# Kernel optimization log

Hardware: AMD Instinct MI355X
Metric: run time of the kernel (lower is better)

Reference implementation:

```python
import jax, jax.numpy as jnp
import numpy as np

B, H, W, C = 2, 128, 128, 192
HEADS = 6
HD = C // HEADS
WS = 16
OWIN = int(WS * 0.5) + WS          # 24
PAD = (OWIN - WS) // 2             # 4
NQ = WS * WS
NK = OWIN * OWIN
EPS = 1e-6
HID = ((int(C * 2.667) + 7) // 8) * 8  # 512


def _rel_pos_index():
    cq = np.stack(np.meshgrid(np.arange(WS), np.arange(WS), indexing='ij')).reshape(2, -1)
    ck = np.stack(np.meshgrid(np.arange(OWIN), np.arange(OWIN), indexing='ij')).reshape(2, -1)
    rel = (ck[:, None, :] - cq[:, :, None]).transpose(1, 2, 0).astype(np.int64)  # (nq, nk, 2)
    rel[:, :, 0] += WS - 1
    rel[:, :, 1] += WS - 1
    rel[:, :, 0] *= WS + OWIN - 1
    return rel.sum(-1)  # (nq, nk)

RPI = jnp.asarray(_rel_pos_index())


def setup_inputs() -> dict:
    key = jax.random.key(0)
    ks = jax.random.split(key, 16)
    def w(k, shape, s=0.02):
        return jax.random.normal(k, shape, jnp.float32) * s
    return {
        'x': jax.random.normal(ks[0], (B, H * W, C), jnp.float32),
        'qkv_w': w(ks[1], (3 * C, C)), 'qkv_b': jnp.zeros((3 * C,), jnp.float32),
        'proj_w': w(ks[2], (C, C)), 'proj_b': jnp.zeros((C,), jnp.float32),
        'rpb': w(ks[3], ((WS + OWIN - 1) ** 2, HEADS)),
        'n1_w': jnp.ones((C,), jnp.float32), 'n1_b': jnp.zeros((C,), jnp.float32),
        'ls1': jnp.full((C,), 1e-6, jnp.float32),
        'n2_w': jnp.ones((C,), jnp.float32), 'n2_b': jnp.zeros((C,), jnp.float32),
        'ls2': jnp.full((C,), 1e-6, jnp.float32),
        'fcgv_w': w(ks[4], (2 * HID, C)), 'fcgv_b': jnp.zeros((2 * HID,), jnp.float32),
        'dw_w': w(ks[5], (HID, 1, 3, 3)), 'dw_b': jnp.zeros((HID,), jnp.float32),
        'dwd_w': w(ks[6], (HID, 1, 3, 3)), 'dwd_b': jnp.zeros((HID,), jnp.float32),
        'dil_scale': w(ks[7], (1,), 0.1),
        'fco_w': w(ks[8], (C, HID)), 'fco_b': jnp.zeros((C,), jnp.float32),
    }


def _iln(x, wgt, bias):
    # spatially-holistic LN: stats over (L, C); returns normed x and residual scale
    xf = x.astype(jnp.float32)
    mean = xf.mean(axis=(1, 2), keepdims=True)
    var = ((xf - mean) ** 2).mean(axis=(1, 2), keepdims=True)
    std = jnp.sqrt(var + EPS)
    scale = jnp.minimum(std, 2.0)  # std_ema buffer initialized to 1.0 (eval path)
    xn = (xf - mean) / scale
    return (xn * wgt + bias).astype(x.dtype), scale


def _oca(x, qkv_w, qkv_b, proj_w, proj_b, rpb):
    b = x.shape[0]
    nh, nw = H // WS, W // WS
    nwin = b * nh * nw
    qkv = x @ qkv_w.T + qkv_b
    q, k, v = jnp.split(qkv, 3, axis=-1)
    # non-overlapping query windows: (nwin, heads, nq, hd)
    qw = q.reshape(b, nh, WS, nw, WS, C).transpose(0, 1, 3, 2, 4, 5)
    qw = qw.reshape(nwin, NQ, HEADS, HD).transpose(0, 2, 1, 3)
    # overlapping K/V windows via unfold(kernel=OWIN, stride=WS, pad=PAD)
    kv = jnp.concatenate([k, v], axis=-1).reshape(b, H, W, 2 * C).transpose(0, 3, 1, 2)
    kvp = jnp.pad(kv, ((0, 0), (0, 0), (PAD, PAD), (PAD, PAD)))
    ih = (jnp.arange(nh) * WS)[:, None] + jnp.arange(OWIN)[None, :]
    iw = (jnp.arange(nw) * WS)[:, None] + jnp.arange(OWIN)[None, :]
    kvw = kvp[:, :, ih][:, :, :, :, iw]               # (b, 2C, nh, owin, nw, owin)
    kvw = kvw.transpose(0, 2, 4, 3, 5, 1).reshape(nwin, NK, 2 * C)
    kw = kvw[..., :C].reshape(nwin, NK, HEADS, HD).transpose(0, 2, 1, 3)
    vw = kvw[..., C:].reshape(nwin, NK, HEADS, HD).transpose(0, 2, 1, 3)
    bias = rpb[RPI].transpose(2, 0, 1)                # (heads, nq, nk)
    logits = jnp.einsum('whqd,whkd->whqk', qw, kw) * (HD ** -0.5) + bias
    attn = jax.nn.softmax(logits, axis=-1)
    out = jnp.einsum('whqk,whkd->whqd', attn, vw)
    out = out.transpose(0, 2, 1, 3).reshape(nwin, NQ, C) @ proj_w.T + proj_b
    # window reverse -> (b, H*W, C)
    out = out.reshape(b, nh, nw, WS, WS, C).transpose(0, 1, 3, 2, 4, 5).reshape(b, H * W, C)
    return out


def _dw(x, wgt, bias, dil):
    y = jax.lax.conv_general_dilated(x, wgt, (1, 1), [(dil, dil), (dil, dil)],
                                     rhs_dilation=(dil, dil), feature_group_count=HID)
    return y + bias[None, :, None, None]


def _ffn(x, fcgv_w, fcgv_b, dw_w, dw_b, dwd_w, dwd_b, dil_scale, fco_w, fco_b):
    gv = x @ fcgv_w.T + fcgv_b
    g, val = jnp.split(gv, 2, axis=-1)
    h = jax.nn.silu(g) * val
    h = h.transpose(0, 2, 1).reshape(-1, HID, H, W)
    h = _dw(h, dw_w, dw_b, 1)
    h = h + dil_scale[0] * _dw(h, dwd_w, dwd_b, 2)
    h = h.reshape(-1, HID, H * W).transpose(0, 2, 1)
    return h @ fco_w.T + fco_b


def reference(x, qkv_w, qkv_b, proj_w, proj_b, rpb, n1_w, n1_b, ls1, n2_w, n2_b, ls2,
              fcgv_w, fcgv_b, dw_w, dw_b, dwd_w, dwd_b, dil_scale, fco_w, fco_b):
    xn, std1 = _iln(x, n1_w, n1_b)
    x = x + std1 * (ls1 * _oca(xn, qkv_w, qkv_b, proj_w, proj_b, rpb))
    xn2, std2 = _iln(x, n2_w, n2_b)
    x = x + std2 * (ls2 * _ffn(xn2, fcgv_w, fcgv_b, dw_w, dw_b, dwd_w, dwd_b, dil_scale, fco_w, fco_b))
    return x
```

## Files before the change

### kernel.cpp

```cpp
#include <hip/hip_runtime.h>

#define DI __device__ __forceinline__

typedef __attribute__((ext_vector_type(8))) short bh8;
typedef __attribute__((ext_vector_type(4))) float fx4;
typedef __attribute__((ext_vector_type(16))) float fx16;

DI short f2bf(float f) {
  unsigned u = __builtin_bit_cast(unsigned, f);
  u += 0x7FFFu + ((u >> 16) & 1u);
  return (short)(u >> 16);
}
DI float bf2f(short s) {
  unsigned u = ((unsigned)(unsigned short)s) << 16;
  return __builtin_bit_cast(float, u);
}
DI fx4 mfma16(bh8 a, bh8 b, fx4 c) {
  return __builtin_amdgcn_mfma_f32_16x16x32_bf16(a, b, c, 0, 0, 0);
}
DI fx16 mfma32(bh8 a, bh8 b, fx16 c) {
  return __builtin_amdgcn_mfma_f32_32x32x16_bf16(a, b, c, 0, 0, 0);
}
DI fx4 fzero() { fx4 z = {0.f, 0.f, 0.f, 0.f}; return z; }

DI float fexp2(float x) {
#if __has_builtin(__builtin_amdgcn_exp2f)
  return __builtin_amdgcn_exp2f(x);
#else
  return exp2f(x);
#endif
}

DI bh8 pack8(const float* src) {
  fx4 v0 = *(const fx4*)src;
  fx4 v1 = *(const fx4*)(src + 4);
  bh8 pk;
#pragma unroll
  for (int j = 0; j < 4; j++) { pk[j] = f2bf(v0[j]); pk[j + 4] = f2bf(v1[j]); }
  return pk;
}
DI bh8 pack8_aff(const float* src, const float* affc) {
  fx4 v0 = *(const fx4*)src;
  fx4 v1 = *(const fx4*)(src + 4);
  bh8 pk;
#pragma unroll
  for (int j = 0; j < 4; j++) {
    pk[j]     = f2bf(v0[j] * affc[2 * j]       + affc[2 * j + 1]);
    pk[j + 4] = f2bf(v1[j] * affc[2 * (j + 4)] + affc[2 * (j + 4) + 1]);
  }
  return pk;
}

__global__ __launch_bounds__(256) void iln_partial(const float* __restrict__ x,
                                                   float* __restrict__ part) {
  const int blk = blockIdx.x, tid = threadIdx.x;
  const fx4* p = (const fx4*)(x + (size_t)blk * 12288);
  float s = 0.f, s2 = 0.f;
#pragma unroll
  for (int i = 0; i < 12; i++) {
    fx4 v = p[i * 256 + tid];
    s  += v[0] + v[1] + v[2] + v[3];
    s2 += v[0] * v[0] + v[1] * v[1] + v[2] * v[2] + v[3] * v[3];
  }
  __shared__ float sm[512];
  sm[tid] = s; sm[256 + tid] = s2;
  __syncthreads();
  for (int st = 128; st > 0; st >>= 1) {
    if (tid < st) { sm[tid] += sm[tid + st]; sm[256 + tid] += sm[256 + tid + st]; }
    __syncthreads();
  }
  if (tid == 0) { part[blk * 2] = sm[0]; part[blk * 2 + 1] = sm[256]; }
}

__global__ __launch_bounds__(256) void iln_final(const float* __restrict__ part,
                                                 const float* __restrict__ w,
                                                 const float* __restrict__ bias,
                                                 float* __restrict__ aff,
                                                 float* __restrict__ st) {
  const int b = blockIdx.x, tid = threadIdx.x;
  __shared__ float sm[512];
  sm[tid]       = part[(b * 256 + tid) * 2];
  sm[256 + tid] = part[(b * 256 + tid) * 2 + 1];
  __syncthreads();
  for (int s = 128; s > 0; s >>= 1) {
    if (tid < s) { sm[tid] += sm[tid + s]; sm[256 + tid] += sm[256 + tid + s]; }
    __syncthreads();
  }
  const float invn = 1.f / 3145728.f;
  float mean = sm[0] * invn;
  float var  = sm[256] * invn - mean * mean;
  float scale = fminf(sqrtf(var + 1e-6f), 2.f);
  if (tid < 192) {
    float a = w[tid] / scale;
    aff[(b * 192 + tid) * 2]     = a;
    aff[(b * 192 + tid) * 2 + 1] = bias[tid] - mean * a;
  }
  if (tid == 0) { st[b * 2] = mean; st[b * 2 + 1] = scale; }
}

__global__ __launch_bounds__(256) void cvt_w(const float* __restrict__ qkv_w,
                                             const float* __restrict__ proj_w,
                                             const float* __restrict__ fcgv_w,
                                             const float* __restrict__ fco_w,
                                             short* __restrict__ wbuf) {
  int t = blockIdx.x * 256 + threadIdx.x;
  int blk = t >> 6, lane = t & 63;
  int g = lane >> 4, h = lane & 15;
  const float* src;
  if (blk < 216) {
    int b2 = blk;
    int ni = b2 % 3; b2 /= 3;
    int wn = b2 & 1; b2 >>= 1;
    int kt = b2 % 6; b2 /= 6;
    int nt = b2;
    src = qkv_w + (size_t)(nt * 96 + wn * 48 + ni * 16 + h) * 192 + kt * 32 + g * 8;
  } else if (blk < 288) {
    int b2 = blk - 216;
    int ni = b2 % 3; b2 /= 3;
    int wn = b2 & 1; b2 >>= 1;
    int kt = b2 % 6; b2 /= 6;
    int nt = b2;
    src = proj_w + (size_t)(nt * 96 + wn * 48 + ni * 16 + h) * 192 + kt * 32 + g * 8;
  } else if (blk < 672) {
    int b2 = blk - 288;
    int gv = b2 & 1; b2 >>= 1;
    int ni = b2 & 1; b2 >>= 1;
    int wn = b2 & 1; b2 >>= 1;
    int kt = b2 % 6; b2 /= 6;
    int nt = b2;
    int r = wn * 32 + ni * 16 + h;
    int row = gv ? (512 + nt * 64 + r) : (nt * 64 + r);
    src = fcgv_w + (size_t)row * 192 + kt * 32 + g * 8;
  } else {
    int b2 = blk - 672;
    int ni = b2 % 3; b2 /= 3;
    int wn = b2 & 1; b2 >>= 1;
    int kt = b2 & 15; b2 >>= 4;
    int nt = b2;
    src = fco_w + (size_t)(nt * 96 + wn * 48 + ni * 16 + h) * 512 + kt * 32 + g * 8;
  }
  *(bh8*)(wbuf + (size_t)blk * 512 + lane * 8) = pack8(src);
}

__global__ __launch_bounds__(256) void cvt_aff(const float* __restrict__ src,
                                               const float* __restrict__ aff,
                                               short* __restrict__ dst) {
  int t = blockIdx.x * 256 + threadIdx.x;
  int row = t / 24;
  int c0 = (t - row * 24) * 8;
  const float* affp = aff + (row >> 14) * 384 + c0 * 2;
  int mt = row >> 7, wm = (row >> 6) & 1, mi = (row >> 4) & 3, h = row & 15;
  int kt = c0 >> 5, g = (c0 >> 3) & 3;
  int blk = ((mt * 2 + wm) * 4 + mi) * 6 + kt;
  int lane = g * 16 + h;
  *(bh8*)(dst + (size_t)blk * 512 + lane * 8) = pack8_aff(src + (size_t)row * 192 + c0, affp);
}

__global__ __launch_bounds__(256) void bias_gen(const float* __restrict__ rpb,
                                                float* __restrict__ btf) {
  int t = blockIdx.x * 256 + threadIdx.x;
  int lane = t & 63;
  int u = t >> 6;
  int qi = u & 1; int u2 = u >> 1;
  int ki = u2 & 1; u2 >>= 1;
  int kc = u2 % 9; u2 = u2 / 9;
  int w = u2 & 3, head = u2 >> 2;
  int c = lane & 31, hi = lane >> 5;
  int q = w * 64 + qi * 32 + c;
  int qterm = (q >> 4) * 39 + (q & 15);
  (void)ki; (void)kc;
  float o[16];
#pragma unroll
  for (int r = 0; r < 16; r++) {
    int kk = ((u >> 2) % 9) * 64 + ((u >> 1) & 1) * 32 + (r & 3) + 8 * (r >> 2) + 4 * hi;
    int ky = (kk * 2731) >> 16;
    int kx = kk - ky * 24;
    int idx = ky * 39 + kx + 600 - qterm;
    o[r] = rpb[idx * 6 + head] * 1.4426950408889634f;
  }
  fx4* dst = (fx4*)btf;
#pragma unroll
  for (int j = 0; j < 4; j++) {
    fx4 v = {o[4 * j], o[4 * j + 1], o[4 * j + 2], o[4 * j + 3]};
    dst[((size_t)u * 4 + j) * 64 + lane] = v;
  }
}

__global__ __launch_bounds__(256) void gemm_qkv(const short* __restrict__ xn,
                                                const short* __restrict__ wq,
                                                const float* __restrict__ wb,
                                                short* __restrict__ qb,
                                                short* __restrict__ kb,
                                                short* __restrict__ vb) {
  const int mt = blockIdx.x, by = blockIdx.y;
  const int m0 = mt * 128;
  const int tid = threadIdx.x, wid = tid >> 6, lane = tid & 63;
  const int g = lane >> 4, h = lane & 15;
  const int wm = wid >> 1, wn = wid & 1;
  fx4 acc[4][3];
#pragma unroll
  for (int i = 0; i < 4; i++)
#pragma unroll
    for (int j = 0; j < 3; j++) acc[i][j] = fzero();

#pragma unroll
  for (int kt = 0; kt < 6; kt++) {
    bh8 af[4], bf[3];
#pragma unroll
    for (int mi = 0; mi < 4; mi++)
      af[mi] = *(const bh8*)(xn + (size_t)((((mt * 2 + wm) * 4 + mi) * 6 + kt)) * 512 + lane * 8);
#pragma unroll
    for (int ni = 0; ni < 3; ni++)
      bf[ni] = *(const bh8*)(wq + (size_t)(((by * 6 + kt) * 2 + wn) * 3 + ni) * 512 + lane * 8);
#pragma unroll
    for (int ni = 0; ni < 3; ni++)
#pragma unroll
      for (int mi = 0; mi < 4; mi++) acc[mi][ni] = mfma16(af[mi], bf[ni], acc[mi][ni]);
  }
  const int seg = by >> 1;
  short* dst = (seg == 0) ? qb : (seg == 1 ? kb : vb);
  const float sc = (seg == 1) ? 0.25503486f : 1.0f;
  const int colbase = (by & 1) * 96;
#pragma unroll
  for (int mi = 0; mi < 4; mi++)
#pragma unroll
    for (int ni = 0; ni < 3; ni++)
#pragma unroll
      for (int r = 0; r < 4; r++) {
        int row = m0 + wm * 64 + mi * 16 + g * 4 + r;
        int col = colbase + wn * 48 + ni * 16 + h;
        dst[(size_t)row * 192 + col] = f2bf((acc[mi][ni][r] + wb[seg * 192 + col]) * sc);
      }
}

__global__ __launch_bounds__(256, 3) void attn_kernel(const short* __restrict__ qb,
                                                      const short* __restrict__ kb,
                                                      const short* __restrict__ vb,
                                                      const float* __restrict__ btf,
                                                      short* __restrict__ ao) {
  __shared__ short K_lds[64 * 40];
  __shared__ short Vt_lds[32 * 72];
  __shared__ float l_lds[256];
  const int tid = threadIdx.x;
  const int win = blockIdx.x, head = blockIdx.y;
  const int b = win >> 6, wy = (win >> 3) & 7, wx = win & 7;
  const int w = tid >> 6, lane = tid & 63, c = lane & 31, hi = lane >> 5;

  bh8 qf[2][2];
#pragma unroll
  for (int qi = 0; qi < 2; qi++) {
    int ql = w * 64 + qi * 32 + c;
    size_t gl = (size_t)(b * 16384 + (wy * 16 + (ql >> 4)) * 128 + wx * 16 + (ql & 15));
#pragma unroll
    for (int ds = 0; ds < 2; ds++)
      qf[qi][ds] = *(const bh8*)(qb + gl * 192 + head * 32 + ds * 16 + hi * 8);
  }
  float l_run[2] = {0.f, 0.f};
  fx16 out[2];
#pragma unroll
  for (int r = 0; r < 16; r++) { out[0][r] = 0.f; out[1][r] = 0.f; }

  const fx4* btf4 = (const fx4*)btf;
  const int hw9 = (head * 4 + w) * 9;

  const int kl_a = tid >> 2, part_a = tid & 3;
  const int kl_b = tid & 63, hg_b = tid >> 6;

  for (int kc = 0; kc < 9; kc++) {
    __syncthreads();
    {
      int key = kc * 64 + kl_a;
      int ky = key / 24, kx = key - ky * 24;
      int py = wy * 16 - 4 + ky, px = wx * 16 - 4 + kx;
      bh8 kv = {};
      if ((unsigned)py < 128u && (unsigned)px < 128u)
        kv = *(const bh8*)(kb + ((size_t)(b * 16384 + py * 128 + px)) * 192 + head * 32 + part_a * 8);
      *(bh8*)&K_lds[kl_a * 40 + part_a * 8] = kv;

      int key2 = kc * 64 + kl_b;
      int ky2 = key2 / 24, kx2 = key2 - ky2 * 24;
      int py2 = wy * 16 - 4 + ky2, px2 = wx * 16 - 4 + kx2;
      bh8 vv = {};
      if ((unsigned)py2 < 128u && (unsigned)px2 < 128u)
        vv = *(const bh8*)(vb + ((size_t)(b * 16384 + py2 * 128 + px2)) * 192 + head * 32 + hg_b * 8);
#pragma unroll
      for (int j = 0; j < 8; j++) Vt_lds[(hg_b * 8 + j) * 72 + kl_b] = vv[j];
    }
    __syncthreads();

    const fx4* base_kc = btf4 + (size_t)(hw9 + kc) * 1024 + lane;
#pragma unroll
    for (int ki = 0; ki < 2; ki++) {
      fx16 st[2];
#pragma unroll
      for (int qi = 0; qi < 2; qi++) {
        const fx4* bp = base_kc + (ki * 2 + qi) * 256;
        fx4 b0 = bp[0], b1 = bp[64], b2 = bp[128], b3 = bp[192];
#pragma unroll
        for (int m = 0; m < 4; m++) {
          st[qi][m]      = b0[m];
          st[qi][4 + m]  = b1[m];
          st[qi][8 + m]  = b2[m];
          st[qi][12 + m] = b3[m];
        }
      }
#pragma unroll
      for (int ds = 0; ds < 2; ds++) {
        bh8 kf = *(bh8*)&K_lds[(ki * 32 + c) * 40 + ds * 16 + hi * 8];
        st[0] = mfma32(kf, qf[0][ds], st[0]);
        st[1] = mfma32(kf, qf[1][ds], st[1]);
      }
#pragma unroll
      for (int qi = 0; qi < 2; qi++) {
        float s = 0.f;
#pragma unroll
        for (int r = 0; r < 16; r++) {
          float p = fexp2(st[qi][r]);
          st[qi][r] = p;
          s += p;
        }
        l_run[qi] += s;
      }
      int dwq[2][2][4];
#pragma unroll
      for (int qi = 0; qi < 2; qi++)
#pragma unroll
        for (int k1 = 0; k1 < 2; k1++)
#pragma unroll
          for (int p01 = 0; p01 < 2; p01++) {
            int rA = 2 * p01 + 8 * k1;
            int A, Bv;
            asm("v_cvt_pk_bf16_f32 %0, %1, %2" : "=v"(A)  : "v"(st[qi][rA]),     "v"(st[qi][rA + 1]));
            asm("v_cvt_pk_bf16_f32 %0, %1, %2" : "=v"(Bv) : "v"(st[qi][rA + 4]), "v"(st[qi][rA + 5]));
#if __has_builtin(__builtin_amdgcn_permlane32_swap)
            auto pr = __builtin_amdgcn_permlane32_swap((unsigned)A, (unsigned)Bv, false, false);
            dwq[qi][k1][p01]     = (int)pr[0];
            dwq[qi][k1][p01 + 2] = (int)pr[1];
#else
            int Ax = __shfl_xor(A, 32);
            int Bx = __shfl_xor(Bv, 32);
            dwq[qi][k1][p01]     = hi ? Bx : A;
            dwq[qi][k1][p01 + 2] = hi ? Bv : Ax;
#endif
          }
#pragma unroll
      for (int k1 = 0; k1 < 2; k1++) {
        bh8 bv2 = *(bh8*)&Vt_lds[c * 72 + (ki * 2 + k1) * 16 + hi * 8];
#pragma unroll
        for (int qi = 0; qi < 2; qi++) {
          int4 t4 = {dwq[qi][k1][0], dwq[qi][k1][1], dwq[qi][k1][2], dwq[qi][k1][3]};
          out[qi] = mfma32(__builtin_bit_cast(bh8, t4), bv2, out[qi]);
        }
      }
    }
  }
#pragma unroll
  for (int qi = 0; qi < 2; qi++) {
    float lp = l_run[qi] + __shfl_xor(l_run[qi], 32);
    l_lds[w * 64 + qi * 32 + c] = 1.f / lp;
  }
  __syncthreads();
#pragma unroll
  for (int qi = 0; qi < 2; qi++)
#pragma unroll
    for (int r = 0; r < 16; r++) {
      int row = (r & 3) + 8 * (r >> 2) + 4 * hi;
      float val = out[qi][r] * l_lds[w * 64 + qi * 32 + row];
      int ql = w * 64 + qi * 32 + row;
      ao[((size_t)(win * 256 + ql)) * 192 + head * 32 + c] = f2bf(val);
    }
}

__global__ __launch_bounds__(256) void gemm_proj(const short* __restrict__ ao,
                                                 const short* __restrict__ wp,
                                                 const float* __restrict__ wb,
                                                 const float* __restrict__ x,
                                                 const float* __restrict__ ls1,
                                                 const float* __restrict__ st,
                                                 float* __restrict__ x1,
                                                 float* __restrict__ part2) {
  __shared__ float red[512];
  const int m0 = blockIdx.x * 128, by = blockIdx.y;
  const int tid = threadIdx.x, wid = tid >> 6, lane = tid & 63;
  const int g = lane >> 4, h = lane & 15;
  const int wm = wid >> 1, wn = wid & 1;
  fx4 acc[4][3];
#pragma unroll
  for (int i = 0; i < 4; i++)
#pragma unroll
    for (int j = 0; j < 3; j++) acc[i][j] = fzero();

#pragma unroll
  for (int kt = 0; kt < 6; kt++) {
    bh8 af[4], bf[3];
#pragma unroll
    for (int mi = 0; mi < 4; mi++)
      af[mi] = *(const bh8*)(ao + (size_t)(m0 + wm * 64 + mi * 16 + h) * 192 + kt * 32 + g * 8);
#pragma unroll
    for (int ni = 0; ni < 3; ni++)
      bf[ni] = *(const bh8*)(wp + (size_t)(((by * 6 + kt) * 2 + wn) * 3 + ni) * 512 + lane * 8);
#pragma unroll
    for (int ni = 0; ni < 3; ni++)
#pragma unroll
      for (int mi = 0; mi < 4; mi++) acc[mi][ni] = mfma16(af[mi], bf[ni], acc[mi][ni]);
  }
  const int n0 = by * 96;
  float ps = 0.f, ps2 = 0.f;
#pragma unroll
  for (int mi = 0; mi < 4; mi++)
#pragma unroll
    for (int ni = 0; ni < 3; ni++)
#pragma unroll
      for (int r = 0; r < 4; r++) {
        int grow = m0 + wm * 64 + mi * 16 + g * 4 + r;
        int win = grow >> 8, q = grow & 255;
        int bb = win >> 6, wy = (win >> 3) & 7, wxx = win & 7;
        int l = (wy * 16 + (q >> 4)) * 128 + wxx * 16 + (q & 15);
        int col = n0 + wn * 48 + ni * 16 + h;
        size_t di = ((size_t)(bb * 16384 + l)) * 192 + col;
        float s1 = st[bb * 2 + 1];
        float val = x[di] + s1 * ls1[col] * (acc[mi][ni][r] + wb[col]);
        x1[di] = val;
        ps += val;
        ps2 += val * val;
      }
  red[tid] = ps; red[256 + tid] = ps2;
  __syncthreads();
  for (int s = 128; s > 0; s >>= 1) {
    if (tid < s) { red[tid] += red[tid + s]; red[256 + tid] += red[256 + tid + s]; }
    __syncthreads();
  }
  if (tid == 0) {
    int pi = blockIdx.x * 2 + by;
    part2[pi * 2] = red[0];
    part2[pi * 2 + 1] = red[256];
  }
}

__global__ __launch_bounds__(256) void gemm_fcgv(const short* __restrict__ x1n,
                                                 const short* __restrict__ wg,
                                                 const float* __restrict__ wb,
                                                 short* __restrict__ hp) {
  __shared__ short T[64 * 136];
  const int mt = blockIdx.x, by = blockIdx.y, n0 = by * 64;
  const int m0 = mt * 128;
  const int b = m0 >> 14, l0 = m0 & 16383;
  const int tid = threadIdx.x, wid = tid >> 6, lane = tid & 63;
  const int g = lane >> 4, h = lane & 15;
  const int wm = wid >> 1, wn = wid & 1;
  fx4 accg[4][2], accv[4][2];
#pragma unroll
  for (int i = 0; i < 4; i++)
#pragma unroll
    for (int j = 0; j < 2; j++) { accg[i][j] = fzero(); accv[i][j] = fzero(); }

#pragma unroll
  for (int kt = 0; kt < 6; kt++) {
    bh8 af[4], bg[2], bv[2];
#pragma unroll
    for (int mi = 0; mi < 4; mi++)
      af[mi] = *(const bh8*)(x1n + (size_t)((((mt * 2 + wm) * 4 + mi) * 6 + kt)) * 512 + lane * 8);
#pragma unroll
    for (int ni = 0; ni < 2; ni++) {
      size_t base = (size_t)((((by * 6 + kt) * 2 + wn) * 2 + ni) * 2) * 512;
      bg[ni] = *(const bh8*)(wg + base + lane * 8);
      bv[ni] = *(const bh8*)(wg + base + 512 + lane * 8);
    }
#pragma unroll
    for (int ni = 0; ni < 2; ni++)
#pragma unroll
      for (int mi = 0; mi < 4; mi++) {
        accg[mi][ni] = mfma16(af[mi], bg[ni], accg[mi][ni]);
        accv[mi][ni] = mfma16(af[mi], bv[ni], accv[mi][ni]);
      }
  }
  short hs[4][2][4];
#pragma unroll
  for (int mi = 0; mi < 4; mi++)
#pragma unroll
    for (int ni = 0; ni < 2; ni++)
#pragma unroll
      for (int r = 0; r < 4; r++) {
        int colg = n0 + wn * 32 + ni * 16 + h;
        float gv = accg[mi][ni][r] + wb[colg];
        float vv = accv[mi][ni][r] + wb[512 + colg];
        hs[mi][ni][r] = f2bf(gv / (1.f + __expf(-gv)) * vv);
      }
#pragma unroll
  for (int mi = 0; mi < 4; mi++)
#pragma unroll
    for (int ni = 0; ni < 2; ni++)
#pragma unroll
      for (int r = 0; r < 4; r++) {
        int cc = wn * 32 + ni * 16 + h;
        int rl = wm * 64 + mi * 16 + g * 4 + r;
        T[cc * 136 + rl] = hs[mi][ni][r];
      }
  __syncthreads();
#pragma unroll
  for (int i = 0; i < 4; i++) {
    int ch = tid + i * 256;
    int cc = ch >> 4, lg = ch & 15;
    bh8 v = *(bh8*)&T[cc * 136 + lg * 8];
    *(bh8*)(hp + (((size_t)(b * 512 + n0 + cc)) << 14) + l0 + lg * 8) = v;
  }
}

__global__ __launch_bounds__(256, 2) void dw_fused(const short* __restrict__ in,
                                                   const float* __restrict__ w1,
                                                   const float* __restrict__ b1,
                                                   const float* __restrict__ w2,
                                                   const float* __restrict__ b2,
                                                   const float* __restrict__ dsc,
                                                   short* __restrict__ outp) {
  __shared__ short P[136 * 128];
  __shared__ short D[136 * 128];
  const int p = blockIdx.x, c = p & 511;
  const int tid = threadIdx.x;
#pragma unroll
  for (int i = 0; i < 8; i++) {
    int gs = i * 256 + tid;
    int yy = gs >> 4, sl = gs & 15;
    bh8 v = *(const bh8*)(in + ((size_t)p << 14) + gs * 8);
    *(bh8*)&P[yy * 136 + sl * 8] = v;
  }
  float k1[9], k2[9];
#pragma unroll
  for (int j = 0; j < 9; j++) { k1[j] = w1[c * 9 + j]; k2[j] = w2[c * 9 + j]; }
  const float bias1 = b1[c], bias2 = b2[c], ds = dsc[0];
  const int y = tid >> 1, hf = tid & 1;
  __syncthreads();

#pragma unroll
  for (int g = 0; g < 8; g++) {
    const int x0 = hf * 64 + g * 8;
    float acc[8];
#pragma unroll
    for (int i = 0; i < 8; i++) acc[i] = bias1;
#pragma unroll
    for (int ky = 0; ky < 3; ky++) {
      int yy = y + ky - 1;
      if ((unsigned)yy < 128u) {
        const short* row = &P[yy * 136];
        float f[10];
        bh8 v = *(const bh8*)&row[x0];
#pragma unroll
        for (int j = 0; j < 8; j++) f[j + 1] = bf2f(v[j]);
        f[0] = (x0 == 0) ? 0.f : bf2f(row[x0 - 1]);
        f[9] = (x0 == 120) ? 0.f : bf2f(row[x0 + 8]);
        float w0 = k1[ky * 3], wA = k1[ky * 3 + 1], wB = k1[ky * 3 + 2];
#pragma unroll
        for (int i = 0; i < 8; i++) acc[i] += f[i] * w0 + f[i + 1] * wA + f[i + 2] * wB;
      }
    }
    bh8 pk;
#pragma unroll
    for (int i = 0; i < 8; i++) pk[i] = f2bf(acc[i]);
    *(bh8*)&D[y * 136 + x0] = pk;
  }
  __syncthreads();

#pragma unroll
  for (int g = 0; g < 8; g++) {
    const int x0 = hf * 64 + g * 8;
    float acc[8], center[8];
#pragma unroll
    for (int i = 0; i < 8; i++) acc[i] = bias2;
#pragma unroll
    for (int ky = 0; ky < 3; ky++) {
      int yy = y + (ky - 1) * 2;
      if ((unsigned)yy < 128u) {
        const short* row = &D[yy * 136];
        float f[12];
        bh8 v = *(const bh8*)&row[x0];
#pragma unroll
        for (int j = 0; j < 8; j++) f[j + 2] = bf2f(v[j]);
        if (x0 == 0) { f[0] = 0.f; f[1] = 0.f; }
        else {
          unsigned lp = *(const unsigned*)&row[x0 - 2];
          f[0] = __builtin_bit_cast(float, lp << 16);
          f[1] = __builtin_bit_cast(float, lp & 0xffff0000u);
        }
        if (x0 == 120) { f[10] = 0.f; f[11] = 0.f; }
        else {
          unsigned rp = *(const unsigned*)&row[x0 + 8];
          f[10] = __builtin_bit_cast(float, rp << 16);
          f[11] = __builtin_bit_cast(float, rp & 0xffff0000u);
        }
        float w0 = k2[ky * 3], wA = k2[ky * 3 + 1], wB = k2[ky * 3 + 2];
#pragma unroll
        for (int i = 0; i < 8; i++) acc[i] += f[i] * w0 + f[i + 2] * wA + f[i + 4] * wB;
        if (ky == 1) {
#pragma unroll
          for (int i = 0; i < 8; i++) center[i] = f[i + 2];
        }
      }
    }
    bh8 pk;
#pragma unroll
    for (int i = 0; i < 8; i++) pk[i] = f2bf(center[i] + ds * acc[i]);
    *(bh8*)(outp + ((size_t)p << 14) + y * 128 + x0) = pk;
  }
}

__global__ __launch_bounds__(256) void gemm_fco(const short* __restrict__ h2,
                                                const short* __restrict__ wo,
                                                const float* __restrict__ wb,
                                                const float* __restrict__ x1,
                                                const float* __restrict__ ls2,
                                                const float* __restrict__ st,
                                                float* __restrict__ out) {
  __shared__ short As[128 * 40];
  const int m0 = blockIdx.x * 128, by = blockIdx.y, n0 = by * 96;
  const int b = m0 >> 14, l0 = m0 & 16383;
  const int tid = threadIdx.x, wid = tid >> 6, lane = tid & 63;
  const int g = lane >> 4, h = lane & 15;
  const int wm = wid >> 1, wn = wid & 1;
  const int cp = tid & 15, lg = tid >> 4;
  fx4 acc[4][3];
#pragma unroll
  for (int i = 0; i < 4; i++)
#pragma unroll
    for (int j = 0; j < 3; j++) acc[i][j] = fzero();

  for (int kt = 0; kt < 16; kt++) {
    const int k0 = kt * 32;
    {
      const short* basep = h2 + (((size_t)(b * 512 + k0 + 2 * cp)) << 14) + l0 + lg * 8;
      bh8 v0 = *(const bh8*)basep;
      bh8 v1 = *(const bh8*)(basep + 16384);
#pragma unroll
      for (int j = 0; j < 8; j++) {
        unsigned pkv = (unsigned)(unsigned short)v0[j] | (((unsigned)(unsigned short)v1[j]) << 16);
        *(unsigned*)&As[(lg * 8 + j) * 40 + 2 * cp] = pkv;
      }
    }
    __syncthreads();
    bh8 af[4], bf[3];
#pragma unroll
    for (int mi = 0; mi < 4; mi++)
      af[mi] = *(bh8*)&As[(wm * 64 + mi * 16 + h) * 40 + g * 8];
#pragma unroll
    for (int ni = 0; ni < 3; ni++)
      bf[ni] = *(const bh8*)(wo + (size_t)(((by * 16 + kt) * 2 + wn) * 3 + ni) * 512 + lane * 8);
#pragma unroll
    for (int ni = 0; ni < 3; ni++)
#pragma unroll
      for (int mi = 0; mi < 4; mi++) acc[mi][ni] = mfma16(af[mi], bf[ni], acc[mi][ni]);
    __syncthreads();
  }
  float s2 = st[b * 2 + 1];
#pragma unroll
  for (int mi = 0; mi < 4; mi++)
#pragma unroll
    for (int ni = 0; ni < 3; ni++)
#pragma unroll
      for (int r = 0; r < 4; r++) {
        int row = m0 + wm * 64 + mi * 16 + g * 4 + r;
        int col = n0 + wn * 48 + ni * 16 + h;
        size_t di = (size_t)row * 192 + col;
        out[di] = x1[di] + s2 * ls2[col] * (acc[mi][ni][r] + wb[col]);
      }
}

extern "C" void kernel_launch(void* const* d_in, const int* in_sizes, int n_in,
                              void* d_out, int out_size, void* d_ws, size_t ws_size,
                              hipStream_t stream) {
  const float* x      = (const float*)d_in[0];
  const float* qkv_w  = (const float*)d_in[1];
  const float* qkv_b  = (const float*)d_in[2];
  const float* proj_w = (const float*)d_in[3];
  const float* proj_b = (const float*)d_in[4];
  const float* rpb    = (const float*)d_in[5];
  const float* n1_w   = (const float*)d_in[6];
  const float* n1_b   = (const float*)d_in[7];
  const float* ls1    = (const float*)d_in[8];
  const float* n2_w   = (const float*)d_in[9];
  const float* n2_b   = (const float*)d_in[10];
  const float* ls2    = (const float*)d_in[11];
  const float* fcgv_w = (const float*)d_in[12];
  const float* fcgv_b = (const float*)d_in[13];
  const float* dw_w   = (const float*)d_in[14];
  const float* dw_b   = (const float*)d_in[15];
  const float* dwd_w  = (const float*)d_in[16];
  const float* dwd_b  = (const float*)d_in[17];
  const float* dil    = (const float*)d_in[18];
  const float* fco_w  = (const float*)d_in[19];
  const float* fco_b  = (const float*)d_in[20];
  float* out = (float*)d_out;
  char* ws = (char*)d_ws;

  short* wbuf = (short*)(ws + 0);
  short* wq = wbuf;
  short* wp = wbuf + 110592;
  short* wg = wbuf + 147456;
  short* wo = wbuf + 344064;
  float* part  = (float*)(ws + 884736);
  float* aff1  = (float*)(ws + 888832);
  float* aff2  = (float*)(ws + 890368);
  float* st1   = (float*)(ws + 891904);
  float* st2   = (float*)(ws + 891968);
  float* part2 = (float*)(ws + 892032);
  short* xn  = (short*)(ws + 1048576);
  float* btf = (float*)(ws + 13631488);
  short* qb  = (short*)(ws + 17301504);
  short* kb  = (short*)(ws + 29884416);
  short* vb  = (short*)(ws + 42467328);
  short* ao  = (short*)(ws + 55050240);
  float* x1  = (float*)(ws + 1048576);
  short* x1n = (short*)(ws + 26214400);
  short* hp  = (short*)(ws + 42467328);

  cvt_w<<<216, 256, 0, stream>>>(qkv_w, proj_w, fcgv_w, fco_w, wbuf);
  iln_partial<<<512, 256, 0, stream>>>(x, part);
  iln_final<<<2, 256, 0, stream>>>(part, n1_w, n1_b, aff1, st1);
  cvt_aff<<<3072, 256, 0, stream>>>(x, aff1, xn);
  bias_gen<<<216, 256, 0, stream>>>(rpb, btf);
  gemm_qkv<<<dim3(256, 6), 256, 0, stream>>>(xn, wq, qkv_b, qb, kb, vb);
  attn_kernel<<<dim3(128, 6), 256, 0, stream>>>(qb, kb, vb, btf, ao);
  gemm_proj<<<dim3(256, 2), 256, 0, stream>>>(ao, wp, proj_b, x, ls1, st1, x1, part2);
  iln_final<<<2, 256, 0, stream>>>(part2, n2_w, n2_b, aff2, st2);
  cvt_aff<<<3072, 256, 0, stream>>>(x1, aff2, x1n);
  gemm_fcgv<<<dim3(256, 8), 256, 0, stream>>>(x1n, wg, fcgv_b, hp);
  dw_fused<<<1024, 256, 0, stream>>>(hp, dw_w, dw_b, dwd_w, dwd_b, dil, hp);
  gemm_fco<<<dim3(256, 2), 256, 0, stream>>>(hp, wo, fco_b, x1, ls2, st2, out);
}
```

Measured before the change: 185.2 us.

## Split depthwise conv planes across two blocks and raise MFMA priority in attention

The fused depthwise-conv kernel now gives each block half of a 128x128 channel plane, loading 3 halo rows for the dilated pass and recomputing the first-conv rows that overlap. This doubles the block count and cuts per-block LDS, so more blocks can be resident. Because neighbouring blocks now read rows the other block writes, the output moves to a separate h2 buffer instead of being written in place. The attention kernel also wraps its MFMA sections in s_setprio to favour matrix-issue waves, at the cost of some redundant halo loads and compute in the conv.

```diff
diff --git a/kernel.cpp b/kernel.cpp
--- a/kernel.cpp
+++ b/kernel.cpp
@@ -304,12 +304,14 @@
           st[qi][12 + m] = b3[m];
         }
       }
+      __builtin_amdgcn_s_setprio(1);
 #pragma unroll
       for (int ds = 0; ds < 2; ds++) {
         bh8 kf = *(bh8*)&K_lds[(ki * 32 + c) * 40 + ds * 16 + hi * 8];
         st[0] = mfma32(kf, qf[0][ds], st[0]);
         st[1] = mfma32(kf, qf[1][ds], st[1]);
       }
+      __builtin_amdgcn_s_setprio(0);
 #pragma unroll
       for (int qi = 0; qi < 2; qi++) {
         float s = 0.f;
@@ -343,6 +345,7 @@
             dwq[qi][k1][p01 + 2] = hi ? Bv : Ax;
 #endif
           }
+      __builtin_amdgcn_s_setprio(1);
 #pragma unroll
       for (int k1 = 0; k1 < 2; k1++) {
         bh8 bv2 = *(bh8*)&Vt_lds[c * 72 + (ki * 2 + k1) * 16 + hi * 8];
@@ -352,6 +355,7 @@
           out[qi] = mfma32(__builtin_bit_cast(bh8, t4), bv2, out[qi]);
         }
       }
+      __builtin_amdgcn_s_setprio(0);
     }
   }
 #pragma unroll
@@ -506,42 +510,46 @@
   }
 }
 
-__global__ __launch_bounds__(256, 2) void dw_fused(const short* __restrict__ in,
-                                                   const float* __restrict__ w1,
-                                                   const float* __restrict__ b1,
-                                                   const float* __restrict__ w2,
-                                                   const float* __restrict__ b2,
-                                                   const float* __restrict__ dsc,
-                                                   short* __restrict__ outp) {
-  __shared__ short P[136 * 128];
-  __shared__ short D[136 * 128];
-  const int p = blockIdx.x, c = p & 511;
+__global__ __launch_bounds__(256) void dw_fused(const short* __restrict__ in,
+                                                const float* __restrict__ w1,
+                                                const float* __restrict__ b1,
+                                                const float* __restrict__ w2,
+                                                const float* __restrict__ b2,
+                                                const float* __restrict__ dsc,
+                                                short* __restrict__ outp) {
+  __shared__ short P[70 * 136];
+  __shared__ short D[68 * 136];
+  const int p = blockIdx.x >> 1, s = blockIdx.x & 1, c = p & 511;
   const int tid = threadIdx.x;
-#pragma unroll
-  for (int i = 0; i < 8; i++) {
-    int gs = i * 256 + tid;
-    int yy = gs >> 4, sl = gs & 15;
-    bh8 v = *(const bh8*)(in + ((size_t)p << 14) + gs * 8);
-    *(bh8*)&P[yy * 136 + sl * 8] = v;
+  const int r0 = s * 64;
+  const int plo = s ? 61 : 0;
+  const int pbase = r0 - 3;
+  const int dlo = s ? 62 : 0;
+  const int dbase = r0 - 2;
+  const short* ip = in + ((size_t)p << 14);
+
+  for (int i = tid; i < 67 * 16; i += 256) {
+    int rr = plo + (i >> 4), sl = i & 15;
+    bh8 v = *(const bh8*)(ip + rr * 128 + sl * 8);
+    *(bh8*)&P[(rr - pbase) * 136 + sl * 8] = v;
   }
   float k1[9], k2[9];
 #pragma unroll
   for (int j = 0; j < 9; j++) { k1[j] = w1[c * 9 + j]; k2[j] = w2[c * 9 + j]; }
   const float bias1 = b1[c], bias2 = b2[c], ds = dsc[0];
-  const int y = tid >> 1, hf = tid & 1;
   __syncthreads();
 
-#pragma unroll
-  for (int g = 0; g < 8; g++) {
-    const int x0 = hf * 64 + g * 8;
+  for (int i = tid; i < 66 * 16; i += 256) {
+    int gy = dlo + (i >> 4);
+    int x0 = (i & 15) * 8;
     float acc[8];
 #pragma unroll
-    for (int i = 0; i < 8; i++) acc[i] = bias1;
+    for (int q = 0; q < 8; q++) acc[q] = bias1;
 #pragma unroll
     for (int ky = 0; ky < 3; ky++) {
-      int yy = y + ky - 1;
+      int yy = gy + ky - 1;
       if ((unsigned)yy < 128u) {
-        const short* row = &P[yy * 136];
+        const short* row = &P[(yy - pbase) * 136];
         float f[10];
         bh8 v = *(const bh8*)&row[x0];
 #pragma unroll
@@ -550,27 +558,27 @@
         f[9] = (x0 == 120) ? 0.f : bf2f(row[x0 + 8]);
         float w0 = k1[ky * 3], wA = k1[ky * 3 + 1], wB = k1[ky * 3 + 2];
 #pragma unroll
-        for (int i = 0; i < 8; i++) acc[i] += f[i] * w0 + f[i + 1] * wA + f[i + 2] * wB;
+        for (int q = 0; q < 8; q++) acc[q] += f[q] * w0 + f[q + 1] * wA + f[q + 2] * wB;
       }
     }
     bh8 pk;
 #pragma unroll
-    for (int i = 0; i < 8; i++) pk[i] = f2bf(acc[i]);
-    *(bh8*)&D[y * 136 + x0] = pk;
+    for (int q = 0; q < 8; q++) pk[q] = f2bf(acc[q]);
+    *(bh8*)&D[(gy - dbase) * 136 + x0] = pk;
   }
   __syncthreads();
 
-#pragma unroll
-  for (int g = 0; g < 8; g++) {
-    const int x0 = hf * 64 + g * 8;
+  for (int i = tid; i < 64 * 16; i += 256) {
+    int gy = r0 + (i >> 4);
+    int x0 = (i & 15) * 8;
     float acc[8], center[8];
 #pragma unroll
-    for (int i = 0; i < 8; i++) acc[i] = bias2;
+    for (int q = 0; q < 8; q++) acc[q] = bias2;
 #pragma unroll
     for (int ky = 0; ky < 3; ky++) {
-      int yy = y + (ky - 1) * 2;
+      int yy = gy + (ky - 1) * 2;
       if ((unsigned)yy < 128u) {
-        const short* row = &D[yy * 136];
+        const short* row = &D[(yy - dbase) * 136];
         float f[12];
         bh8 v = *(const bh8*)&row[x0];
 #pragma unroll
@@ -589,17 +597,17 @@
         }
         float w0 = k2[ky * 3], wA = k2[ky * 3 + 1], wB = k2[ky * 3 + 2];
 #pragma unroll
-        for (int i = 0; i < 8; i++) acc[i] += f[i] * w0 + f[i + 2] * wA + f[i + 4] * wB;
+        for (int q = 0; q < 8; q++) acc[q] += f[q] * w0 + f[q + 2] * wA + f[q + 4] * wB;
         if (ky == 1) {
 #pragma unroll
-          for (int i = 0; i < 8; i++) center[i] = f[i + 2];
+          for (int q = 0; q < 8; q++) center[q] = f[q + 2];
         }
       }
     }
     bh8 pk;
 #pragma unroll
-    for (int i = 0; i < 8; i++) pk[i] = f2bf(center[i] + ds * acc[i]);
-    *(bh8*)(outp + ((size_t)p << 14) + y * 128 + x0) = pk;
+    for (int q = 0; q < 8; q++) pk[q] = f2bf(center[q] + ds * acc[q]);
+    *(bh8*)(outp + ((size_t)p << 14) + gy * 128 + x0) = pk;
   }
 }
 
@@ -710,6 +718,7 @@
   float* x1  = (float*)(ws + 1048576);
   short* x1n = (short*)(ws + 26214400);
   short* hp  = (short*)(ws + 42467328);
+  short* h2  = (short*)(ws + 76021760);
 
   cvt_w<<<216, 256, 0, stream>>>(qkv_w, proj_w, fcgv_w, fco_w, wbuf);
   iln_partial<<<512, 256, 0, stream>>>(x, part);
@@ -722,6 +731,6 @@
   iln_final<<<2, 256, 0, stream>>>(part2, n2_w, n2_b, aff2, st2);
   cvt_aff<<<3072, 256, 0, stream>>>(x1, aff2, x1n);
   gemm_fcgv<<<dim3(256, 8), 256, 0, stream>>>(x1n, wg, fcgv_b, hp);
-  dw_fused<<<1024, 256, 0, stream>>>(hp, dw_w, dw_b, dwd_w, dwd_b, dil, hp);
-  gemm_fco<<<dim3(256, 2), 256, 0, stream>>>(hp, wo, fco_b, x1, ls2, st2, out);
-}
+  dw_fused<<<2048, 256, 0, stream>>>(hp, dw_w, dw_b, dwd_w, dwd_b, dil, h2);
+  gemm_fco<<<dim3(256, 2), 256, 0, stream>>>(h2, wo, fco_b, x1, ls2, st2, out);
+}
```

Result: no change. 186.7 us (median of 2 runs) (+0.8%).
